# Performance work log

Measured on AMD Instinct MI355X. Metric: run time of the kernel, lower is better.

The kernel has to match this reference:

```python
import jax, jax.numpy as jnp
import numpy as np

B_SZ, L, D_MODEL = 2, 2048, 1024
EXPAND, N_STATE, K = 2, 16, 4
D_INNER = D_MODEL * EXPAND


def setup_inputs() -> dict:
    key = jax.random.key(0)
    ks = jax.random.split(key, 12)
    s = lambda k, shape, scale=0.02: jax.random.normal(k, shape, jnp.float32) * scale
    return {
        "x": jax.random.normal(ks[0], (B_SZ, L, D_MODEL), jnp.float32),
        "ln_gamma": jnp.ones((D_MODEL,), jnp.float32),
        "ln_beta": jnp.zeros((D_MODEL,), jnp.float32),
        "W_in": s(ks[1], (D_MODEL, 2 * D_INNER)),
        "conv_w": s(ks[2], (D_INNER, 1, K), 0.1),
        "conv_b": jnp.zeros((D_INNER,), jnp.float32),
        "A_log": jax.random.normal(ks[3], (N_STATE,), jnp.float32),
        "B_mat": s(ks[4], (N_STATE, D_INNER), 0.05),
        "C_mat": s(ks[5], (D_INNER, N_STATE), 0.05),
        "D_vec": s(ks[6], (D_INNER,), 0.1),
        "Wd": s(ks[7], (D_INNER, D_INNER)),
        "bd": jnp.zeros((D_INNER,), jnp.float32),
        "W_out": s(ks[8], (D_INNER, D_MODEL)),
    }


def _layernorm(x, g, b, eps=1e-5):
    mu = jnp.mean(x, axis=-1, keepdims=True)
    var = jnp.var(x, axis=-1, keepdims=True)
    return (x - mu) * jax.lax.rsqrt(var + eps) * g + b


def _selective_scan(x, delta, A, B_mat, C_mat, D_vec):
    # x: (b,l,d), delta: (b,l), A: (n,)
    dA = jnp.exp(delta[..., None] * A)            # (b,l,n)
    Bx = jnp.einsum('bld,nd->bln', x, B_mat) * delta[..., None]  # (b,l,n)

    def step(h, inp):
        dA_t, Bx_t = inp
        h = dA_t * h + Bx_t
        return h, h

    h0 = jnp.zeros((x.shape[0], A.shape[0]), x.dtype)
    # scan over seq axis
    _, hs = jax.lax.scan(step, h0, (jnp.swapaxes(dA, 0, 1), jnp.swapaxes(Bx, 0, 1)))
    hs = jnp.swapaxes(hs, 0, 1)                   # (b,l,n)
    return jnp.einsum('bln,dn->bld', hs, C_mat) + D_vec * x


def reference(x, ln_gamma, ln_beta, W_in, conv_w, conv_b, A_log, B_mat, C_mat, D_vec, Wd, bd, W_out):
    residual = x
    h = _layernorm(x, ln_gamma, ln_beta)
    xg = h @ W_in                                  # (b,l,2*d_inner)
    xs, gate = jnp.split(xg, 2, axis=-1)
    # depthwise causal conv (torch pads K-1 both sides then slices [:L] == left pad K-1)
    xc = jnp.swapaxes(xs, 1, 2)                    # (b,d,l)
    xc = jax.lax.conv_general_dilated(
        xc, conv_w, window_strides=(1,), padding=((K - 1, 0),),
        dimension_numbers=('NCH', 'OIH', 'NCH'), feature_group_count=D_INNER)
    xc = xc + conv_b[None, :, None]
    xs = jnp.swapaxes(xc, 1, 2)                    # (b,l,d)
    xs = jax.nn.silu(xs)
    # S4 kernel
    delta = jnp.mean(jax.nn.softplus(xs @ Wd + bd), axis=-1)  # (b,l)
    A = -jnp.exp(A_log)
    y = _selective_scan(xs, delta, A, B_mat, C_mat, D_vec)
    y = y * jax.nn.silu(gate)
    y = y @ W_out
    return residual + y
```

## Files before the change

### kernel.cpp

```cpp
#include <hip/hip_runtime.h>
#include <cstdint>
#include <cstddef>

typedef unsigned short u16;
typedef __attribute__((ext_vector_type(4))) float floatx4;
typedef __attribute__((ext_vector_type(8))) __bf16 bf16x8;

__device__ __forceinline__ float u2f(u16 u) {
    union { unsigned int i; float f; } x;
    x.i = ((unsigned int)u) << 16;
    return x.f;
}
__device__ __forceinline__ u16 f2u(float f) {
    union { float f; unsigned int i; } x;
    x.f = f;
    unsigned int r = x.i + 0x7fffu + ((x.i >> 16) & 1u);
    return (u16)(r >> 16);
}

__device__ __forceinline__ void swz(int bid, int& x, int& y) {
    int xcd = bid & 7;
    int lid = bid >> 3;
    x = lid >> 2;
    y = xcd * 4 + (lid & 3);
}

__device__ __forceinline__ void tr_tile(const float* __restrict__ in, u16* __restrict__ out,
                                        int K, int N, int bx, int by, float* tile ) {
    int n0 = bx * 32, k0 = by * 32;
    int t = threadIdx.x;
    int r = t >> 3, c4 = (t & 7) * 4;
    float4 v = *(const float4*)(in + (size_t)(k0 + r) * N + n0 + c4);
    tile[r * 33 + c4 + 0] = v.x;
    tile[r * 33 + c4 + 1] = v.y;
    tile[r * 33 + c4 + 2] = v.z;
    tile[r * 33 + c4 + 3] = v.w;
    __syncthreads();
    int n = t >> 3, kg = (t & 7) * 4;
    ushort4 o;
    o.x = f2u(tile[(kg + 0) * 33 + n]);
    o.y = f2u(tile[(kg + 1) * 33 + n]);
    o.z = f2u(tile[(kg + 2) * 33 + n]);
    o.w = f2u(tile[(kg + 3) * 33 + n]);
    *(ushort4*)(out + (size_t)(n0 + n) * K + k0 + kg) = o;
}

__global__ __launch_bounds__(256)
void prep_kernel(const float* __restrict__ W_in, u16* __restrict__ Wt_in,
                 const float* __restrict__ Wd, u16* __restrict__ Wt_ext,
                 const float* __restrict__ W_out, u16* __restrict__ Wt_out,
                 const float* __restrict__ B_mat,
                 const float* __restrict__ x, const float* __restrict__ gamma,
                 const float* __restrict__ beta, u16* __restrict__ h,
                 float* __restrict__ out) {
    __shared__ float tile[32 * 33];
    int blk = blockIdx.x, t = threadIdx.x;
    if (blk < 4096) {
        tr_tile(W_in, Wt_in, 1024, 4096, blk & 127, blk >> 7, tile);
    } else if (blk < 8192) {
        int b2 = blk - 4096;
        tr_tile(Wd, Wt_ext, 2048, 2048, b2 & 63, b2 >> 6, tile);
    } else if (blk < 10240) {
        int b3 = blk - 8192;
        tr_tile(W_out, Wt_out, 2048, 1024, b3 & 31, b3 >> 5, tile);
    } else if (blk < 14336) {
        int r = blk - 10240;
        const float4* xr = (const float4*)(x + (size_t)r * 1024);
        float4 xv = xr[t];
        ((float4*)(out + (size_t)r * 1024))[t] = xv;
        float s = xv.x + xv.y + xv.z + xv.w;
        float ss = xv.x * xv.x + xv.y * xv.y + xv.z * xv.z + xv.w * xv.w;
#pragma unroll
        for (int off = 32; off > 0; off >>= 1) {
            s += __shfl_down(s, off, 64);
            ss += __shfl_down(ss, off, 64);
        }
        __shared__ float rs[4], rss[4], mu_s, ri_s;
        int wave = t >> 6, lane = t & 63;
        if (lane == 0) { rs[wave] = s; rss[wave] = ss; }
        __syncthreads();
        if (t == 0) {
            float S = rs[0] + rs[1] + rs[2] + rs[3];
            float SS = rss[0] + rss[1] + rss[2] + rss[3];
            float mu = S * (1.f / 1024.f);
            float var = SS * (1.f / 1024.f) - mu * mu;
            mu_s = mu;
            ri_s = rsqrtf(fmaxf(var, 0.f) + 1e-5f);
        }
        __syncthreads();
        float mu = mu_s, ri = ri_s;
        float4 gv = ((const float4*)gamma)[t];
        float4 bv = ((const float4*)beta)[t];
        ushort4 o;
        o.x = f2u((xv.x - mu) * ri * gv.x + bv.x);
        o.y = f2u((xv.y - mu) * ri * gv.y + bv.y);
        o.z = f2u((xv.z - mu) * ri * gv.z + bv.z);
        o.w = f2u((xv.w - mu) * ri * gv.w + bv.w);
        ((ushort4*)(h + (size_t)r * 1024))[t] = o;
    } else {
        int idx = (blk - 14336) * 256 + t;
        int row = 2048 + (idx >> 11), col = idx & 2047;
        u16 v = (row < 2064) ? f2u(B_mat[(size_t)(row - 2048) * 2048 + col]) : (u16)0;
        Wt_ext[(size_t)row * 2048 + col] = v;
    }
}

__device__ __forceinline__ void gl_lds16(const u16* g, u16* l) {
    __builtin_amdgcn_global_load_lds(
        (const __attribute__((address_space(1))) void*)g,
        (__attribute__((address_space(3))) void*)l, 16, 0, 0);
}

template <int EPI>
__device__ __forceinline__
void gemm128_body(const u16* __restrict__ A, const u16* __restrict__ Bt,
                  void* __restrict__ out, int M, int N, int K, int Ksub) {
    __shared__ u16 As[128 * 64];
    __shared__ u16 Bs[128 * 64];
    int bx, by;
    swz(blockIdx.x, bx, by);
    const int tid = threadIdx.x;
    const int wave = tid >> 6, lane = tid & 63;
    const int row0 = by * 128, col0 = bx * 128;
    const int koff = blockIdx.y * Ksub;
    const int l16 = lane & 15, q = lane >> 4;
    const int sRow = lane >> 2, sK = (lane & 3) * 8;

    floatx4 acc[4][4];
#pragma unroll
    for (int i = 0; i < 4; ++i)
#pragma unroll
        for (int j = 0; j < 4; ++j) acc[i][j] = (floatx4){0.f, 0.f, 0.f, 0.f};

    const u16* gA = A + (size_t)(row0 + wave * 32 + sRow) * K + koff + sK;
    const u16* gB = Bt + (size_t)(col0 + wave * 32 + sRow) * K + koff + sK;
    u16* lA = As + wave * 1024;
    u16* lB = Bs + wave * 1024;
    const int rowb = (wave >> 1) * 64, colb = (wave & 1) * 64;

    for (int k0 = 0; k0 < Ksub; k0 += 64) {
#pragma unroll
        for (int h = 0; h < 2; ++h) {
            gl_lds16(gA + h * 32, lA + h * 4096);
            gl_lds16(gA + (size_t)16 * K + h * 32, lA + h * 4096 + 512);
            gl_lds16(gB + h * 32, lB + h * 4096);
            gl_lds16(gB + (size_t)16 * K + h * 32, lB + h * 4096 + 512);
        }
        gA += 64; gB += 64;
        __syncthreads();
#pragma unroll
        for (int h = 0; h < 2; ++h) {
            bf16x8 af[4], bfr[4];
#pragma unroll
            for (int mi = 0; mi < 4; ++mi)
                af[mi] = *(const bf16x8*)(As + h * 4096 + (rowb + mi * 16 + l16) * 32 + q * 8);
#pragma unroll
            for (int ni = 0; ni < 4; ++ni)
                bfr[ni] = *(const bf16x8*)(Bs + h * 4096 + (colb + ni * 16 + l16) * 32 + q * 8);
#pragma unroll
            for (int mi = 0; mi < 4; ++mi)
#pragma unroll
                for (int ni = 0; ni < 4; ++ni)
                    acc[mi][ni] = __builtin_amdgcn_mfma_f32_16x16x32_bf16(
                        af[mi], bfr[ni], acc[mi][ni], 0, 0, 0);
        }
        __syncthreads();
    }

    const int mB = row0 + rowb;
    const int nB = col0 + colb + l16;
    if constexpr (EPI == 0) {
        u16* o = (u16*)out;
#pragma unroll
        for (int mi = 0; mi < 4; ++mi)
#pragma unroll
            for (int ni = 0; ni < 4; ++ni)
#pragma unroll
                for (int rr = 0; rr < 4; ++rr)
                    o[(size_t)(mB + mi * 16 + q * 4 + rr) * N + nB + ni * 16] =
                        f2u(acc[mi][ni][rr]);
    } else {
        float* C = (float*)out;
#pragma unroll
        for (int mi = 0; mi < 4; ++mi)
#pragma unroll
            for (int ni = 0; ni < 4; ++ni)
#pragma unroll
                for (int rr = 0; rr < 4; ++rr)
                    atomicAdd(&C[(size_t)(mB + mi * 16 + q * 4 + rr) * N + nB + ni * 16],
                              acc[mi][ni][rr]);
    }
}

__global__ __launch_bounds__(256)
void gemm_xg(const u16* __restrict__ A, const u16* __restrict__ Bt,
             u16* __restrict__ out, int M, int N, int K) {
    gemm128_body<0>(A, Bt, out, M, N, K, K);
}

__global__ __launch_bounds__(256)
void gemm_fin(const u16* __restrict__ A, const u16* __restrict__ Bt,
              void* __restrict__ out, int M, int N, int K, int Ksub) {
    gemm128_body<4>(A, Bt, out, M, N, K, Ksub);
}

__global__ __launch_bounds__(256)
void gemm_fin_pl(const u16* __restrict__ A, const u16* __restrict__ Bt,
                 u16* __restrict__ planes, int M, int N, int K, int Ksub) {
    u16* plane = planes + (size_t)blockIdx.y * M * N;
    gemm128_body<0>(A, Bt, plane, M, N, K, Ksub);
}

__global__ __launch_bounds__(256)
void fin_reduce(const u16* __restrict__ planes, float* __restrict__ out) {
    const size_t PL = (size_t)4096 * 1024;
    const size_t idx = ((size_t)blockIdx.x * 256 + threadIdx.x) * 8;
    float acc[8] = {0.f, 0.f, 0.f, 0.f, 0.f, 0.f, 0.f, 0.f};
#pragma unroll
    for (int p = 0; p < 4; ++p) {
        ushort4 v0 = *(const ushort4*)(planes + p * PL + idx);
        ushort4 v1 = *(const ushort4*)(planes + p * PL + idx + 4);
        acc[0] += u2f(v0.x); acc[1] += u2f(v0.y); acc[2] += u2f(v0.z); acc[3] += u2f(v0.w);
        acc[4] += u2f(v1.x); acc[5] += u2f(v1.y); acc[6] += u2f(v1.z); acc[7] += u2f(v1.w);
    }
    float4 o0 = *(const float4*)(out + idx);
    float4 o1 = *(const float4*)(out + idx + 4);
    o0.x += acc[0]; o0.y += acc[1]; o0.z += acc[2]; o0.w += acc[3];
    o1.x += acc[4]; o1.y += acc[5]; o1.z += acc[6]; o1.w += acc[7];
    *(float4*)(out + idx) = o0;
    *(float4*)(out + idx + 4) = o1;
}

__global__ __launch_bounds__(256)
void gemm_delta_sk(const u16* __restrict__ A, const u16* __restrict__ Bt,
                   u16* __restrict__ planes, int M, int N, int K, int Ksub) {
    u16* plane = planes + (size_t)blockIdx.y * M * N;
    gemm128_body<0>(A, Bt, plane, M, N, K, Ksub);
}

__global__ __launch_bounds__(256)
void delta_reduce(const u16* __restrict__ planes, const float* __restrict__ bias,
                  float* __restrict__ dacc, float* __restrict__ Bdotn) {
    const int r = blockIdx.x;
    const int t = threadIdx.x;
    const size_t PL = (size_t)4096 * 2176;
    const u16* p0 = planes + (size_t)r * 2176 + t * 8;
    const u16* p1 = p0 + PL;
    ushort4 a0 = *(const ushort4*)p0;
    ushort4 a1 = *(const ushort4*)(p0 + 4);
    ushort4 b0 = *(const ushort4*)p1;
    ushort4 b1 = *(const ushort4*)(p1 + 4);
    float4 c0 = *(const float4*)(bias + t * 8);
    float4 c1 = *(const float4*)(bias + t * 8 + 4);
    float e[8];
    e[0] = u2f(a0.x) + u2f(b0.x) + c0.x;
    e[1] = u2f(a0.y) + u2f(b0.y) + c0.y;
    e[2] = u2f(a0.z) + u2f(b0.z) + c0.z;
    e[3] = u2f(a0.w) + u2f(b0.w) + c0.w;
    e[4] = u2f(a1.x) + u2f(b1.x) + c1.x;
    e[5] = u2f(a1.y) + u2f(b1.y) + c1.y;
    e[6] = u2f(a1.z) + u2f(b1.z) + c1.z;
    e[7] = u2f(a1.w) + u2f(b1.w) + c1.w;
    float sv = 0.f;
#pragma unroll
    for (int i = 0; i < 8; ++i)
        sv += (e[i] > 20.f) ? e[i] : log1pf(expf(e[i]));
#pragma unroll
    for (int off = 32; off > 0; off >>= 1)
        sv += __shfl_down(sv, off, 64);
    __shared__ float wsum[4];
    const int wave = t >> 6, lane = t & 63;
    if (lane == 0) wsum[wave] = sv;
    __syncthreads();
    if (t == 0) dacc[r] = wsum[0] + wsum[1] + wsum[2] + wsum[3];
    if (t < 16) {
        const u16* q = planes + (size_t)r * 2176 + 2048 + t;
        Bdotn[(size_t)t * 4096 + r] = u2f(*q) + u2f(*(q + PL));
    }
}

__global__ __launch_bounds__(256)
void gemm_delta(const u16* __restrict__ A, const u16* __restrict__ Bt,
                float* __restrict__ dacc, const float* __restrict__ bias,
                float* __restrict__ Bdotn, int M, int N, int K) {
    __shared__ u16 As[128 * 128];
    __shared__ u16 Bs[64 * 128];
    int bx, by;
    swz(blockIdx.x, bx, by);
    const int tid = threadIdx.x;
    const int wave = tid >> 6, lane = tid & 63;
    const int row0 = by * 128, col0 = bx * 64;
    const int l16 = lane & 15, q = lane >> 4;
    const int sRow = lane >> 2, sK = (lane & 3) * 8;

    floatx4 acc[2][4];
#pragma unroll
    for (int i = 0; i < 2; ++i)
#pragma unroll
        for (int j = 0; j < 4; ++j) acc[i][j] = (floatx4){0.f, 0.f, 0.f, 0.f};

    const u16* gA = A + (size_t)(row0 + wave * 32 + sRow) * K + sK;
    const u16* gB = Bt + (size_t)(col0 + wave * 16 + sRow) * K + sK;
    u16* lA = As + wave * 1024;
    u16* lB = Bs + wave * 512;
    const int rowb = wave * 32;

    for (int k0 = 0; k0 < K; k0 += 128) {
#pragma unroll
        for (int h = 0; h < 4; ++h) {
            gl_lds16(gA + h * 32, lA + h * 4096);
            gl_lds16(gA + (size_t)16 * K + h * 32, lA + h * 4096 + 512);
            gl_lds16(gB + h * 32, lB + h * 2048);
        }
        gA += 128; gB += 128;
        __syncthreads();
#pragma unroll
        for (int h = 0; h < 4; ++h) {
            bf16x8 af[2], bfr[4];
#pragma unroll
            for (int mi = 0; mi < 2; ++mi)
                af[mi] = *(const bf16x8*)(As + h * 4096 + (rowb + mi * 16 + l16) * 32 + q * 8);
#pragma unroll
            for (int ni = 0; ni < 4; ++ni)
                bfr[ni] = *(const bf16x8*)(Bs + h * 2048 + (ni * 16 + l16) * 32 + q * 8);
#pragma unroll
            for (int mi = 0; mi < 2; ++mi)
#pragma unroll
                for (int ni = 0; ni < 4; ++ni)
                    acc[mi][ni] = __builtin_amdgcn_mfma_f32_16x16x32_bf16(
                        af[mi], bfr[ni], acc[mi][ni], 0, 0, 0);
        }
        __syncthreads();
    }

    const int mB = row0 + rowb;
    const int nB = col0 + l16;
    if (col0 < 2048) {
#pragma unroll
        for (int mi = 0; mi < 2; ++mi) {
#pragma unroll
            for (int rr = 0; rr < 4; ++rr) {
                float sv = 0.f;
#pragma unroll
                for (int ni = 0; ni < 4; ++ni) {
                    float t2 = acc[mi][ni][rr] + bias[nB + ni * 16];
                    sv += (t2 > 20.f) ? t2 : log1pf(expf(t2));
                }
#pragma unroll
                for (int off = 1; off < 16; off <<= 1)
                    sv += __shfl_xor(sv, off, 64);
                if (l16 == 0)
                    atomicAdd(&dacc[mB + mi * 16 + q * 4 + rr], sv);
            }
        }
    } else {
#pragma unroll
        for (int mi = 0; mi < 2; ++mi)
#pragma unroll
            for (int rr = 0; rr < 4; ++rr)
                Bdotn[(size_t)l16 * 4096 + mB + mi * 16 + q * 4 + rr] =
                    acc[mi][0][rr];
    }
}

__global__ __launch_bounds__(256) void conv_silu_kernel(const u16* __restrict__ xg,
                                                        const float* __restrict__ conv_w,
                                                        const float* __restrict__ conv_b,
                                                        u16* __restrict__ xsc,
                                                        float* __restrict__ delta_acc) {
    int r0 = blockIdx.x * 4;
    int l0 = r0 & 2047, bb = r0 >> 11;
    int t = threadIdx.x, d8 = t * 8;
    if (t < 4) delta_acc[r0 + t] = 0.f;

    ushort4 rw[7][2];
#pragma unroll
    for (int j = 0; j < 7; ++j) {
        int ls = l0 + j - 3;
        if (ls >= 0) {
            const u16* row = xg + (size_t)((bb << 11) + ls) * 4096 + d8;
            rw[j][0] = *(const ushort4*)row;
            rw[j][1] = *(const ushort4*)(row + 4);
        } else {
            rw[j][0] = (ushort4){0, 0, 0, 0};
            rw[j][1] = (ushort4){0, 0, 0, 0};
        }
    }
    float w[8][4];
#pragma unroll
    for (int j = 0; j < 8; ++j) {
        float4 wv = *(const float4*)(conv_w + (size_t)(d8 + j) * 4);
        w[j][0] = wv.x; w[j][1] = wv.y; w[j][2] = wv.z; w[j][3] = wv.w;
    }
    float cb[8];
    {
        float4 b0 = *(const float4*)(conv_b + d8);
        float4 b1 = *(const float4*)(conv_b + d8 + 4);
        cb[0] = b0.x; cb[1] = b0.y; cb[2] = b0.z; cb[3] = b0.w;
        cb[4] = b1.x; cb[5] = b1.y; cb[6] = b1.z; cb[7] = b1.w;
    }
#pragma unroll
    for (int i = 0; i < 4; ++i) {
        float xs[8];
#pragma unroll
        for (int j = 0; j < 8; ++j) xs[j] = cb[j];
#pragma unroll
        for (int k = 0; k < 4; ++k) {
            ushort4 u0 = rw[i + k][0], u1 = rw[i + k][1];
            xs[0] += w[0][k] * u2f(u0.x); xs[1] += w[1][k] * u2f(u0.y);
            xs[2] += w[2][k] * u2f(u0.z); xs[3] += w[3][k] * u2f(u0.w);
            xs[4] += w[4][k] * u2f(u1.x); xs[5] += w[5][k] * u2f(u1.y);
            xs[6] += w[6][k] * u2f(u1.z); xs[7] += w[7][k] * u2f(u1.w);
        }
        ushort4 o0, o1;
        o0.x = f2u(xs[0] / (1.f + expf(-xs[0])));
        o0.y = f2u(xs[1] / (1.f + expf(-xs[1])));
        o0.z = f2u(xs[2] / (1.f + expf(-xs[2])));
        o0.w = f2u(xs[3] / (1.f + expf(-xs[3])));
        o1.x = f2u(xs[4] / (1.f + expf(-xs[4])));
        o1.y = f2u(xs[5] / (1.f + expf(-xs[5])));
        o1.z = f2u(xs[6] / (1.f + expf(-xs[6])));
        o1.w = f2u(xs[7] / (1.f + expf(-xs[7])));
        u16* orow = xsc + (size_t)(r0 + i) * 2048 + d8;
        *(ushort4*)orow = o0;
        *(ushort4*)(orow + 4) = o1;
    }
}

__global__ __launch_bounds__(256) void scan_kernel(const float* __restrict__ delta_acc,
                                                   const float* __restrict__ Bdotn,
                                                   const float* __restrict__ A_log,
                                                   float* __restrict__ hsn) {
    int chain = blockIdx.x;
    int b = chain >> 4, n = chain & 15;
    int t = threadIdx.x;
    int wave = t >> 6, lane = t & 63;
    __shared__ float sd[2048], sb[2048];
    __shared__ float wA[4], wB[4];
#pragma unroll
    for (int m = 0; m < 2; ++m) {
        int idx = (m * 256 + t) * 4;
        *(float4*)(sd + idx) = *(const float4*)(delta_acc + b * 2048 + idx);
        *(float4*)(sb + idx) = *(const float4*)(Bdotn + (size_t)n * 4096 + b * 2048 + idx);
    }
    __syncthreads();
    float An = -expf(A_log[n]);
    int base = t * 8;
    float a[8], bb[8];
#pragma unroll
    for (int i = 0; i < 8; ++i) {
        float dl = sd[base + i] * (1.f / 2048.f);
        a[i] = expf(dl * An);
        bb[i] = sb[base + i] * dl;
    }
    float Aacc = 1.f, Bacc = 0.f;
#pragma unroll
    for (int i = 0; i < 8; ++i) {
        Bacc = a[i] * Bacc + bb[i];
        Aacc = a[i] * Aacc;
    }
#pragma unroll
    for (int d = 1; d < 64; d <<= 1) {
        float Ap = __shfl_up(Aacc, d, 64);
        float Bp = __shfl_up(Bacc, d, 64);
        if (lane >= d) {
            Bacc = Aacc * Bp + Bacc;
            Aacc = Aacc * Ap;
        }
    }
    if (lane == 63) { wA[wave] = Aacc; wB[wave] = Bacc; }
    float eA = __shfl_up(Aacc, 1, 64);
    float eB = __shfl_up(Bacc, 1, 64);
    if (lane == 0) { eA = 1.f; eB = 0.f; }
    __syncthreads();
    float pB = 0.f;
#pragma unroll
    for (int w = 0; w < 3; ++w)
        if (w < wave) pB = wA[w] * pB + wB[w];
    float h = eA * pB + eB;
#pragma unroll
    for (int i = 0; i < 8; ++i) {
        h = a[i] * h + bb[i];
        sd[base + i] = h;
    }
    __syncthreads();
#pragma unroll
    for (int m = 0; m < 2; ++m) {
        int idx = (m * 256 + t) * 4;
        *(float4*)(hsn + (size_t)n * 4096 + b * 2048 + idx) = *(const float4*)(sd + idx);
    }
}

__global__ __launch_bounds__(256) void ymid_kernel(const float* __restrict__ hsn,
                                                   const float* __restrict__ C_mat,
                                                   const float* __restrict__ D_vec,
                                                   const u16* __restrict__ xsc,
                                                   const u16* __restrict__ xg,
                                                   u16* __restrict__ ymid) {
    const int t = threadIdx.x;
    const int d0 = blockIdx.x * 512 + t * 2;
    const int r0 = blockIdx.y * 16;
    __shared__ float hsv[16 * 16];
    {
        int rl = t >> 4, nn = t & 15;
        hsv[t] = hsn[(size_t)nn * 4096 + r0 + rl];
    }
    float c0[16], c1[16];
#pragma unroll
    for (int k = 0; k < 4; ++k) {
        float4 v0 = *(const float4*)(C_mat + (size_t)d0 * 16 + k * 4);
        float4 v1 = *(const float4*)(C_mat + (size_t)(d0 + 1) * 16 + k * 4);
        c0[k * 4 + 0] = v0.x; c0[k * 4 + 1] = v0.y; c0[k * 4 + 2] = v0.z; c0[k * 4 + 3] = v0.w;
        c1[k * 4 + 0] = v1.x; c1[k * 4 + 1] = v1.y; c1[k * 4 + 2] = v1.z; c1[k * 4 + 3] = v1.w;
    }
    const float dv0 = D_vec[d0], dv1 = D_vec[d0 + 1];
    __syncthreads();
#pragma unroll 4
    for (int rl = 0; rl < 16; ++rl) {
        const int r = r0 + rl;
        float h0 = 0.f, h1 = 0.f;
#pragma unroll
        for (int nn = 0; nn < 16; ++nn) {
            float hv = hsv[rl * 16 + nn];
            h0 += hv * c0[nn];
            h1 += hv * c1[nn];
        }
        unsigned int xv = *(const unsigned int*)(xsc + (size_t)r * 2048 + d0);
        unsigned int gv = *(const unsigned int*)(xg + (size_t)r * 4096 + 2048 + d0);
        float x0 = u2f((u16)(xv & 0xffffu)), x1 = u2f((u16)(xv >> 16));
        float g0 = u2f((u16)(gv & 0xffffu)), g1 = u2f((u16)(gv >> 16));
        float y0 = (h0 + dv0 * x0) * (g0 / (1.f + expf(-g0)));
        float y1 = (h1 + dv1 * x1) * (g1 / (1.f + expf(-g1)));
        unsigned int o = (unsigned int)f2u(y0) | ((unsigned int)f2u(y1) << 16);
        *(unsigned int*)(ymid + (size_t)r * 2048 + d0) = o;
    }
}

extern "C" void kernel_launch(void* const* d_in, const int* in_sizes, int n_in,
                              void* d_out, int out_size, void* d_ws, size_t ws_size,
                              hipStream_t stream) {
    (void)in_sizes; (void)n_in;
    const float* x      = (const float*)d_in[0];
    const float* ln_g   = (const float*)d_in[1];
    const float* ln_b   = (const float*)d_in[2];
    const float* W_in   = (const float*)d_in[3];
    const float* conv_w = (const float*)d_in[4];
    const float* conv_b = (const float*)d_in[5];
    const float* A_log  = (const float*)d_in[6];
    const float* B_mat  = (const float*)d_in[7];
    const float* C_mat  = (const float*)d_in[8];
    const float* D_vec  = (const float*)d_in[9];
    const float* Wd     = (const float*)d_in[10];
    const float* bd     = (const float*)d_in[11];
    const float* W_out  = (const float*)d_in[12];
    float* out = (float*)d_out;

    char* base = (char*)d_ws;
    u16* Wt_in  = (u16*)base;
    u16* h_ln   = (u16*)base + 4096ull * 1024;
    u16* ymid   = (u16*)base;
    u16* Wt_ext = (u16*)(base + (16ull << 20));
    u16* Wt_out = (u16*)(base + (25ull << 20));
    u16* xg     = (u16*)(base + (29ull << 20));
    u16* xsc    = (u16*)(base + (61ull << 20));
    float* delta_acc = (float*)(base + (77ull << 20));
    float* Bdotn = delta_acc + 4096;
    float* hsn   = Bdotn + 16 * 4096;
    u16* planes  = (u16*)(base + (78ull << 20));
    u16* fplanes = (u16*)(base + (78ull << 20));
    size_t needed = (77ull << 20) + 4096ull * 4 * (1 + 2 * 16);
    size_t needed_sk = (78ull << 20) + 2ull * 4096 * 2176 * 2;

    if (needed > ws_size) {
        hipMemsetAsync(d_out, 0x7F, (size_t)out_size * 4, stream);
        return;
    }
    const bool use_sk = (ws_size >= needed_sk);

    prep_kernel<<<14848, 256, 0, stream>>>(W_in, Wt_in, Wd, Wt_ext, W_out, Wt_out,
                                           B_mat, x, ln_g, ln_b, h_ln, out);
    gemm_xg<<<1024, 256, 0, stream>>>(h_ln, Wt_in, xg, 4096, 4096, 1024);
    conv_silu_kernel<<<1024, 256, 0, stream>>>(xg, conv_w, conv_b, xsc, delta_acc);
    if (use_sk) {
        gemm_delta_sk<<<dim3(544, 2), 256, 0, stream>>>(xsc, Wt_ext, planes,
                                                        4096, 2176, 2048, 1024);
        delta_reduce<<<4096, 256, 0, stream>>>(planes, bd, delta_acc, Bdotn);
    } else {
        gemm_delta<<<1056, 256, 0, stream>>>(xsc, Wt_ext, delta_acc, bd, Bdotn,
                                             4096, 2112, 2048);
    }
    scan_kernel<<<32, 256, 0, stream>>>(delta_acc, Bdotn, A_log, hsn);
    ymid_kernel<<<dim3(4, 256), 256, 0, stream>>>(hsn, C_mat, D_vec, xsc, xg, ymid);
    if (use_sk) {
        gemm_fin_pl<<<dim3(256, 4), 256, 0, stream>>>(ymid, Wt_out, fplanes,
                                                      4096, 1024, 2048, 512);
        fin_reduce<<<2048, 256, 0, stream>>>(fplanes, out);
    } else {
        gemm_fin<<<dim3(256, 2), 256, 0, stream>>>(ymid, Wt_out, out, 4096, 1024, 2048, 1024);
    }
}
```

Before: 325.5 us.

## Replace input projection GEMM with 256x256 tile, 8-wave double-buffered kernel

Swaps the 128x128 single-buffered input projection GEMM for a new kernel that computes 256x256 tiles with 512 threads and double-buffered LDS. Global-to-LDS loads for the next k-tile are interleaved with the current tile's MFMA phases, and s_setprio boosts the math phases. The larger tile raises arithmetic intensity and data reuse per block. The costs are 128 KB of LDS per block, only 256 blocks on the device, and many barriers per k-tile.

```diff
diff --git a/kernel.cpp b/kernel.cpp
--- a/kernel.cpp
+++ b/kernel.cpp
@@ -111,6 +111,149 @@
         (__attribute__((address_space(3))) void*)l, 16, 0, 0);
 }
 
+template <int CB, int NB>
+__device__ __forceinline__
+void ktile256(u16 (&As)[2][16384], u16 (&Bs)[2][16384],
+              const u16* __restrict__ gA, const u16* __restrict__ gB,
+              int kt, bool doStage, int K,
+              int w, int wr, int wc, int l16, int q,
+              floatx4 (&acc)[8][4]) {
+    asm volatile("s_waitcnt vmcnt(0)" ::: "memory");
+    __builtin_amdgcn_s_barrier();
+    asm volatile("" ::: "memory");
+    bf16x8 af[4][2], bfr[4][2];
+    const int aBase = wr * 128, bBase = wc * 64;
+#pragma unroll
+    for (int i = 0; i < 4; ++i)
+#pragma unroll
+        for (int h = 0; h < 2; ++h)
+            af[i][h] = *(const bf16x8*)&As[CB][h * 8192 + (aBase + i * 16 + l16) * 32 + q * 8];
+#pragma unroll
+    for (int j = 0; j < 2; ++j)
+#pragma unroll
+        for (int h = 0; h < 2; ++h)
+            bfr[j][h] = *(const bf16x8*)&Bs[CB][h * 8192 + (bBase + j * 16 + l16) * 32 + q * 8];
+    if (doStage) {
+        const u16* p = gA + (size_t)(kt + 1) * 64;
+#pragma unroll
+        for (int h = 0; h < 2; ++h) {
+            gl_lds16(p + h * 32,                  &As[NB][h * 8192 + w * 1024]);
+            gl_lds16(p + (size_t)16 * K + h * 32, &As[NB][h * 8192 + w * 1024 + 512]);
+        }
+    }
+    __builtin_amdgcn_s_barrier();
+    __builtin_amdgcn_s_setprio(1);
+#pragma unroll
+    for (int i = 0; i < 4; ++i)
+#pragma unroll
+        for (int j = 0; j < 2; ++j)
+#pragma unroll
+            for (int h = 0; h < 2; ++h)
+                acc[i][j] = __builtin_amdgcn_mfma_f32_16x16x32_bf16(af[i][h], bfr[j][h], acc[i][j], 0, 0, 0);
+    __builtin_amdgcn_s_setprio(0);
+    __builtin_amdgcn_s_barrier();
+#pragma unroll
+    for (int j = 2; j < 4; ++j)
+#pragma unroll
+        for (int h = 0; h < 2; ++h)
+            bfr[j][h] = *(const bf16x8*)&Bs[CB][h * 8192 + (bBase + j * 16 + l16) * 32 + q * 8];
+    if (doStage) {
+        const u16* p = gB + (size_t)(kt + 1) * 64;
+#pragma unroll
+        for (int h = 0; h < 2; ++h) {
+            gl_lds16(p + h * 32,                  &Bs[NB][h * 8192 + w * 1024]);
+            gl_lds16(p + (size_t)16 * K + h * 32, &Bs[NB][h * 8192 + w * 1024 + 512]);
+        }
+    }
+    __builtin_amdgcn_s_barrier();
+    __builtin_amdgcn_s_setprio(1);
+#pragma unroll
+    for (int i = 0; i < 4; ++i)
+#pragma unroll
+        for (int j = 2; j < 4; ++j)
+#pragma unroll
+            for (int h = 0; h < 2; ++h)
+                acc[i][j] = __builtin_amdgcn_mfma_f32_16x16x32_bf16(af[i][h], bfr[j][h], acc[i][j], 0, 0, 0);
+    __builtin_amdgcn_s_setprio(0);
+    __builtin_amdgcn_s_barrier();
+#pragma unroll
+    for (int i = 0; i < 4; ++i)
+#pragma unroll
+        for (int h = 0; h < 2; ++h)
+            af[i][h] = *(const bf16x8*)&As[CB][h * 8192 + (aBase + (4 + i) * 16 + l16) * 32 + q * 8];
+    __builtin_amdgcn_s_barrier();
+    __builtin_amdgcn_s_setprio(1);
+#pragma unroll
+    for (int i = 0; i < 4; ++i)
+#pragma unroll
+        for (int j = 0; j < 2; ++j)
+#pragma unroll
+            for (int h = 0; h < 2; ++h)
+                acc[4 + i][j] = __builtin_amdgcn_mfma_f32_16x16x32_bf16(af[i][h], bfr[j][h], acc[4 + i][j], 0, 0, 0);
+    __builtin_amdgcn_s_setprio(0);
+    __builtin_amdgcn_s_barrier();
+    __builtin_amdgcn_s_setprio(1);
+#pragma unroll
+    for (int i = 0; i < 4; ++i)
+#pragma unroll
+        for (int j = 2; j < 4; ++j)
+#pragma unroll
+            for (int h = 0; h < 2; ++h)
+                acc[4 + i][j] = __builtin_amdgcn_mfma_f32_16x16x32_bf16(af[i][h], bfr[j][h], acc[4 + i][j], 0, 0, 0);
+    __builtin_amdgcn_s_setprio(0);
+    __builtin_amdgcn_s_barrier();
+}
+
+__global__ __launch_bounds__(512, 2)
+void gemm_xg256(const u16* __restrict__ A, const u16* __restrict__ Bt,
+                u16* __restrict__ out, int M, int N, int K) {
+    __shared__ u16 As[2][16384];
+    __shared__ u16 Bs[2][16384];
+    const int bid = blockIdx.x;
+    const int xcd = bid & 7, lid = bid >> 3;
+    const int by = xcd * 2 + (lid & 1), bx = lid >> 1;
+    const int tid = threadIdx.x;
+    const int w = tid >> 6, lane = tid & 63;
+    const int wr = w >> 2, wc = w & 3;
+    const int row0 = by * 256, col0 = bx * 256;
+    const int l16 = lane & 15, q = lane >> 4;
+    const int sRow = lane >> 2, sK = (lane & 3) * 8;
+
+    floatx4 acc[8][4];
+#pragma unroll
+    for (int i = 0; i < 8; ++i)
+#pragma unroll
+        for (int j = 0; j < 4; ++j) acc[i][j] = (floatx4){0.f, 0.f, 0.f, 0.f};
+
+    const u16* gA = A + (size_t)(row0 + w * 32 + sRow) * K + sK;
+    const u16* gB = Bt + (size_t)(col0 + w * 32 + sRow) * K + sK;
+
+#pragma unroll
+    for (int h = 0; h < 2; ++h) {
+        gl_lds16(gA + h * 32,                  &As[0][h * 8192 + w * 1024]);
+        gl_lds16(gA + (size_t)16 * K + h * 32, &As[0][h * 8192 + w * 1024 + 512]);
+        gl_lds16(gB + h * 32,                  &Bs[0][h * 8192 + w * 1024]);
+        gl_lds16(gB + (size_t)16 * K + h * 32, &Bs[0][h * 8192 + w * 1024 + 512]);
+    }
+
+    const int nkt = K >> 6;
+    for (int t2 = 0; t2 < nkt; t2 += 2) {
+        ktile256<0, 1>(As, Bs, gA, gB, t2, true, K, w, wr, wc, l16, q, acc);
+        ktile256<1, 0>(As, Bs, gA, gB, t2 + 1, (t2 + 2) < nkt, K, w, wr, wc, l16, q, acc);
+    }
+
+    const int mB = row0 + wr * 128;
+    const int nB = col0 + wc * 64 + l16;
+#pragma unroll
+    for (int mi = 0; mi < 8; ++mi)
+#pragma unroll
+        for (int ni = 0; ni < 4; ++ni)
+#pragma unroll
+            for (int rr = 0; rr < 4; ++rr)
+                out[(size_t)(mB + mi * 16 + q * 4 + rr) * N + nB + ni * 16] =
+                    f2u(acc[mi][ni][rr]);
+}
+
 template <int EPI>
 __device__ __forceinline__
 void gemm128_body(const u16* __restrict__ A, const u16* __restrict__ Bt,
@@ -190,12 +333,6 @@
                     atomicAdd(&C[(size_t)(mB + mi * 16 + q * 4 + rr) * N + nB + ni * 16],
                               acc[mi][ni][rr]);
     }
-}
-
-__global__ __launch_bounds__(256)
-void gemm_xg(const u16* __restrict__ A, const u16* __restrict__ Bt,
-             u16* __restrict__ out, int M, int N, int K) {
-    gemm128_body<0>(A, Bt, out, M, N, K, K);
 }
 
 __global__ __launch_bounds__(256)
@@ -274,8 +411,8 @@
     __syncthreads();
     if (t == 0) dacc[r] = wsum[0] + wsum[1] + wsum[2] + wsum[3];
     if (t < 16) {
-        const u16* q = planes + (size_t)r * 2176 + 2048 + t;
-        Bdotn[(size_t)t * 4096 + r] = u2f(*q) + u2f(*(q + PL));
+        const u16* qp = planes + (size_t)r * 2176 + 2048 + t;
+        Bdotn[(size_t)t * 4096 + r] = u2f(*qp) + u2f(*(qp + PL));
     }
 }
 
@@ -579,7 +716,7 @@
 
     prep_kernel<<<14848, 256, 0, stream>>>(W_in, Wt_in, Wd, Wt_ext, W_out, Wt_out,
                                            B_mat, x, ln_g, ln_b, h_ln, out);
-    gemm_xg<<<1024, 256, 0, stream>>>(h_ln, Wt_in, xg, 4096, 4096, 1024);
+    gemm_xg256<<<256, 512, 0, stream>>>(h_ln, Wt_in, xg, 4096, 4096, 1024);
     conv_silu_kernel<<<1024, 256, 0, stream>>>(xg, conv_w, conv_b, xsc, delta_acc);
     if (use_sk) {
         gemm_delta_sk<<<dim3(544, 2), 256, 0, stream>>>(xsc, Wt_ext, planes,
```

Result: faster. 314.2 us (-3.5%).
